# Performance work log

Measured on AMD Instinct MI355X. Metric: run time of the kernel, lower is better.

Reference implementation:

```python
import jax, jax.numpy as jnp
import numpy as np

EMPTY = -100.0
# class_relation_dict from init_kwargs (int keys)
CLASS_RELATIONS = {0: [1, 2], 1: [0, 3], 2: [4, 5], 3: [6, 7],
                   4: [0, 1], 5: [2, 3], 6: [4, 5], 7: [6, 0]}


def setup_inputs() -> dict:
    key = jax.random.key(0)
    B, C, D, H, W = 8, 8, 128, 128, 128
    x = jax.random.normal(key, (B, C, D, H, W), dtype=jnp.float32)
    # Make some class channels fully 'empty' so the mask-inference path fires
    # (randn alone never equals EMPTY exactly, which would make the op a no-op).
    x = x.at[:4, 0].set(EMPTY)
    x = x.at[2:6, 3].set(EMPTY)
    x = x.at[5:, 6].set(EMPTY)
    return {"x": x}


def reference(x):
    # x: [B, C, D, H, W]
    is_empty = x == EMPTY                       # [B, C, D, H, W] bool
    red_axes = tuple(range(2, x.ndim))
    all_empty = jnp.all(is_empty, axis=red_axes)   # [B, C] channel fully unlabeled
    has_empty = jnp.any(is_empty, axis=red_axes)   # [B, C] channel has any unlabeled voxel

    bshape = (-1,) + (1,) * (x.ndim - 2)  # broadcast [B] -> [B,1,1,1]
    out = jnp.full_like(x, EMPTY)
    for c, rel in CLASS_RELATIONS.items():
        # union of positives over related channels that are themselves fully labeled
        pos = jnp.zeros((x.shape[0],) + x.shape[2:], dtype=bool)
        for ind in rel:
            valid = (~has_empty[:, ind]).reshape(bshape)  # related channel fully labeled
            pos = pos | (valid & (x[:, ind] > 0))
        cond = all_empty[:, c].reshape(bshape) & pos
        out = out.at[:, c].set(jnp.where(cond, 0.0, EMPTY))
    return out
```

## Files before the change

### kernel.cpp

```cpp
#include <hip/hip_runtime.h>
#include <stdint.h>

#define EMPTY_VAL (-100.0f)

typedef float f4 __attribute__((ext_vector_type(4)));

constexpr int B = 8, C = 8;
constexpr int VOX       = 128 * 128 * 128;
constexpr int CH_VEC4   = VOX / 4;
constexpr int THREADS   = 256;
constexpr int ITERS     = 8;
constexpr int V4_PER_BLOCK    = THREADS * ITERS;
constexpr int BLOCKS_PER_BATCH = CH_VEC4 / V4_PER_BLOCK;
constexpr int GRID      = B * BLOCKS_PER_BATCH;

constexpr int REL0c[8] = {1, 0, 4, 6, 0, 2, 4, 6};
constexpr int REL1c[8] = {2, 3, 5, 7, 1, 3, 5, 0};

__global__ __launch_bounds__(THREADS) void mask_kernel(
    const float* __restrict__ x, uint32_t* __restrict__ mask,
    int* __restrict__ flagsE, int* __restrict__ flagsN) {
  const int b     = blockIdx.x / BLOCKS_PER_BATCH;
  const int chunk = blockIdx.x % BLOCKS_PER_BATCH;
  const int tid   = threadIdx.x;
  const size_t vb4 = (size_t)chunk * V4_PER_BLOCK;

  const f4* xb = reinterpret_cast<const f4*>(x) + (size_t)b * C * CH_VEC4;
  uint32_t* mb = mask + (size_t)b * CH_VEC4;

  uint32_t anyE = 0, anyN = 0;

  for (int it = 0; it < ITERS; ++it) {
    const size_t i4 = vb4 + (size_t)it * THREADS + tid;
    uint32_t m = 0;
#pragma unroll
    for (int c = 0; c < C; ++c) {
      const f4 v = __builtin_nontemporal_load(xb + ((size_t)c * CH_VEC4 + i4));
      uint32_t pos = (v.x > 0.f ? 0x00000001u : 0u) |
                     (v.y > 0.f ? 0x00000100u : 0u) |
                     (v.z > 0.f ? 0x00010000u : 0u) |
                     (v.w > 0.f ? 0x01000000u : 0u);
      m |= pos << c;
      const bool e0 = (v.x == EMPTY_VAL), e1 = (v.y == EMPTY_VAL);
      const bool e2 = (v.z == EMPTY_VAL), e3 = (v.w == EMPTY_VAL);
      if (e0 | e1 | e2 | e3)             anyE |= (1u << c);
      if ((!e0) | (!e1) | (!e2) | (!e3)) anyN |= (1u << c);
    }
    __builtin_nontemporal_store(m, mb + i4);
  }

#pragma unroll
  for (int o = 32; o > 0; o >>= 1) {
    anyE |= __shfl_xor((int)anyE, o);
    anyN |= __shfl_xor((int)anyN, o);
  }
  __shared__ int sE, sN;
  if (tid == 0) { sE = 0; sN = 0; }
  __syncthreads();
  if ((tid & 63) == 0) {
    if (anyE) atomicOr(&sE, (int)anyE);
    if (anyN) atomicOr(&sN, (int)anyN);
  }
  __syncthreads();
  if (tid == 0) {
    if (sE) atomicOr(&flagsE[b], sE);
    if (sN) atomicOr(&flagsN[b], sN);
  }
}

__global__ __launch_bounds__(THREADS) void emit_kernel(
    const uint32_t* __restrict__ mask, const int* __restrict__ flagsE,
    const int* __restrict__ flagsN, float* __restrict__ out) {
  const int b     = blockIdx.x / BLOCKS_PER_BATCH;
  const int chunk = blockIdx.x % BLOCKS_PER_BATCH;
  const int tid   = threadIdx.x;

  const int fE = flagsE[b], fN = flagsN[b];

  uint32_t relmask[C];
#pragma unroll
  for (int c = 0; c < C; ++c) {
    const bool all_empty = ((fN >> c) & 1) == 0;
    uint32_t rm = 0;
    if (all_empty) {
      if (((fE >> REL0c[c]) & 1) == 0) rm |= 1u << REL0c[c];
      if (((fE >> REL1c[c]) & 1) == 0) rm |= 1u << REL1c[c];
    }
    relmask[c] = rm * 0x01010101u;
  }

  const size_t vb4 = (size_t)chunk * V4_PER_BLOCK;
  const uint32_t* mb = mask + (size_t)b * CH_VEC4;
  f4* ob = reinterpret_cast<f4*>(out) + (size_t)b * C * CH_VEC4;

  for (int it = 0; it < ITERS; ++it) {
    const size_t i4 = vb4 + (size_t)it * THREADS + tid;
    const uint32_t m = mb[i4];
#pragma unroll
    for (int c = 0; c < C; ++c) {
      const uint32_t t = m & relmask[c];
      f4 r;
      r.x = (t & 0x000000ffu) ? 0.f : EMPTY_VAL;
      r.y = (t & 0x0000ff00u) ? 0.f : EMPTY_VAL;
      r.z = (t & 0x00ff0000u) ? 0.f : EMPTY_VAL;
      r.w = (t & 0xff000000u) ? 0.f : EMPTY_VAL;
      __builtin_nontemporal_store(r, ob + ((size_t)c * CH_VEC4 + i4));
    }
  }
}

constexpr int FB_V4_PER_THREAD = 16;
constexpr int FB_BLOCK_VEC4    = THREADS * FB_V4_PER_THREAD;
constexpr int FB_BLOCKS_PER_CH = CH_VEC4 / FB_BLOCK_VEC4;
constexpr int NCH              = B * C;
constexpr int FB_TOTAL_BLOCKS  = NCH * FB_BLOCKS_PER_CH;

__global__ __launch_bounds__(THREADS) void fb_flags_kernel(
    const float* __restrict__ x, int* __restrict__ flags) {
  const int blk   = blockIdx.x;
  const int ch    = blk / FB_BLOCKS_PER_CH;
  const int chunk = blk % FB_BLOCKS_PER_CH;
  const int tid   = threadIdx.x;
  const float4* p = reinterpret_cast<const float4*>(x) +
                    (size_t)ch * CH_VEC4 + (size_t)chunk * FB_BLOCK_VEC4;
  bool any_empty = false, any_nonempty = false;
#pragma unroll
  for (int i = 0; i < FB_V4_PER_THREAD; ++i) {
    float4 v = p[tid + i * THREADS];
    const bool e0 = (v.x == EMPTY_VAL), e1 = (v.y == EMPTY_VAL);
    const bool e2 = (v.z == EMPTY_VAL), e3 = (v.w == EMPTY_VAL);
    any_empty    |= (e0 | e1 | e2 | e3);
    any_nonempty |= (!e0 | !e1 | !e2 | !e3);
  }
  const bool we = __any(any_empty);
  const bool wn = __any(any_nonempty);
  __shared__ int s_e, s_n;
  if (tid == 0) { s_e = 0; s_n = 0; }
  __syncthreads();
  if ((tid & 63) == 0) {
    if (we) atomicOr(&s_e, 1);
    if (wn) atomicOr(&s_n, 1);
  }
  __syncthreads();
  if (tid == 0) {
    if (s_e) atomicOr(&flags[ch * 2 + 0], 1);
    if (s_n) atomicOr(&flags[ch * 2 + 1], 1);
  }
}

__global__ __launch_bounds__(THREADS) void fb_out_kernel(
    const float* __restrict__ x, const int* __restrict__ flags,
    float* __restrict__ out) {
  const int blk   = blockIdx.x;
  const int ch    = blk / FB_BLOCKS_PER_CH;
  const int chunk = blk % FB_BLOCKS_PER_CH;
  const int b     = ch >> 3;
  const int c     = ch & 7;
  const int tid   = threadIdx.x;
  const size_t base = (size_t)ch * CH_VEC4 + (size_t)chunk * FB_BLOCK_VEC4;
  float4* o = reinterpret_cast<float4*>(out) + base;
  const float4 empty4 = make_float4(EMPTY_VAL, EMPTY_VAL, EMPTY_VAL, EMPTY_VAL);
  const bool all_empty = (flags[ch * 2 + 1] == 0);
  if (!all_empty) {
#pragma unroll
    for (int i = 0; i < FB_V4_PER_THREAD; ++i) o[tid + i * THREADS] = empty4;
    return;
  }
  const int r0 = REL0c[c], r1 = REL1c[c];
  const bool v0 = (flags[(b * 8 + r0) * 2 + 0] == 0);
  const bool v1 = (flags[(b * 8 + r1) * 2 + 0] == 0);
  if (!v0 && !v1) {
#pragma unroll
    for (int i = 0; i < FB_V4_PER_THREAD; ++i) o[tid + i * THREADS] = empty4;
    return;
  }
  const float4* p0 = reinterpret_cast<const float4*>(x) +
                     ((size_t)(b * 8 + r0) * CH_VEC4 + (size_t)chunk * FB_BLOCK_VEC4);
  const float4* p1 = reinterpret_cast<const float4*>(x) +
                     ((size_t)(b * 8 + r1) * CH_VEC4 + (size_t)chunk * FB_BLOCK_VEC4);
  const float4 zero4 = make_float4(0.f, 0.f, 0.f, 0.f);
#pragma unroll
  for (int i = 0; i < FB_V4_PER_THREAD; ++i) {
    const int idx = tid + i * THREADS;
    const float4 a = v0 ? p0[idx] : zero4;
    const float4 q = v1 ? p1[idx] : zero4;
    float4 r;
    r.x = (a.x > 0.f || q.x > 0.f) ? 0.f : EMPTY_VAL;
    r.y = (a.y > 0.f || q.y > 0.f) ? 0.f : EMPTY_VAL;
    r.z = (a.z > 0.f || q.z > 0.f) ? 0.f : EMPTY_VAL;
    r.w = (a.w > 0.f || q.w > 0.f) ? 0.f : EMPTY_VAL;
    o[idx] = r;
  }
}

extern "C" void kernel_launch(void* const* d_in, const int* in_sizes, int n_in,
                              void* d_out, int out_size, void* d_ws, size_t ws_size,
                              hipStream_t stream) {
  const float* x = (const float*)d_in[0];
  float* out     = (float*)d_out;

  const size_t mask_bytes = (size_t)B * CH_VEC4 * sizeof(uint32_t);
  if (ws_size >= mask_bytes + 64) {
    uint32_t* mask = (uint32_t*)d_ws;
    int* flagsE    = (int*)((char*)d_ws + mask_bytes);
    int* flagsN    = flagsE + 8;
    (void)hipMemsetAsync(flagsE, 0, 16 * sizeof(int), stream);
    mask_kernel<<<GRID, THREADS, 0, stream>>>(x, mask, flagsE, flagsN);
    emit_kernel<<<GRID, THREADS, 0, stream>>>(mask, flagsE, flagsN, out);
  } else {
    int* flags = (int*)d_ws;
    (void)hipMemsetAsync(flags, 0, NCH * 2 * sizeof(int), stream);
    fb_flags_kernel<<<FB_TOTAL_BLOCKS, THREADS, 0, stream>>>(x, flags);
    fb_out_kernel<<<FB_TOTAL_BLOCKS, THREADS, 0, stream>>>(x, flags, out);
  }
}
```

Before: 215.7 us.

## Fuse mask and emit passes into one cooperative kernel with grid sync

```diff
diff --git a/kernel.cpp b/kernel.cpp
--- a/kernel.cpp
+++ b/kernel.cpp
@@ -1,4 +1,5 @@
 #include <hip/hip_runtime.h>
+#include <hip/hip_cooperative_groups.h>
 #include <stdint.h>
 
 #define EMPTY_VAL (-100.0f)
@@ -6,31 +7,32 @@
 typedef float f4 __attribute__((ext_vector_type(4)));
 
 constexpr int B = 8, C = 8;
-constexpr int VOX       = 128 * 128 * 128;
-constexpr int CH_VEC4   = VOX / 4;
-constexpr int THREADS   = 256;
-constexpr int ITERS     = 8;
-constexpr int V4_PER_BLOCK    = THREADS * ITERS;
-constexpr int BLOCKS_PER_BATCH = CH_VEC4 / V4_PER_BLOCK;
-constexpr int GRID      = B * BLOCKS_PER_BATCH;
+constexpr int VOX     = 128 * 128 * 128;
+constexpr int CH_VEC4 = VOX / 4;
+constexpr int THREADS = 256;
 
 constexpr int REL0c[8] = {1, 0, 4, 6, 0, 2, 4, 6};
 constexpr int REL1c[8] = {2, 3, 5, 7, 1, 3, 5, 0};
 
-__global__ __launch_bounds__(THREADS) void mask_kernel(
-    const float* __restrict__ x, uint32_t* __restrict__ mask,
-    int* __restrict__ flagsE, int* __restrict__ flagsN) {
-  const int b     = blockIdx.x / BLOCKS_PER_BATCH;
-  const int chunk = blockIdx.x % BLOCKS_PER_BATCH;
+constexpr int ITERS_F   = 16;
+constexpr int V4_BLK_F  = THREADS * ITERS_F;
+constexpr int BPB_F     = CH_VEC4 / V4_BLK_F;
+constexpr int GRID_F    = B * BPB_F;
+
+__global__ __launch_bounds__(THREADS, 4) void fused_kernel(
+    const float* __restrict__ x, int* __restrict__ flagsE,
+    int* __restrict__ flagsN, float* __restrict__ out) {
+  const int b     = blockIdx.x / BPB_F;
+  const int chunk = blockIdx.x % BPB_F;
   const int tid   = threadIdx.x;
-  const size_t vb4 = (size_t)chunk * V4_PER_BLOCK;
+  const size_t vb4 = (size_t)chunk * V4_BLK_F;
 
   const f4* xb = reinterpret_cast<const f4*>(x) + (size_t)b * C * CH_VEC4;
-  uint32_t* mb = mask + (size_t)b * CH_VEC4;
-
+
+  __shared__ uint32_t lds_m[V4_BLK_F];
   uint32_t anyE = 0, anyN = 0;
 
-  for (int it = 0; it < ITERS; ++it) {
+  for (int it = 0; it < ITERS_F; ++it) {
     const size_t i4 = vb4 + (size_t)it * THREADS + tid;
     uint32_t m = 0;
 #pragma unroll
@@ -46,7 +48,7 @@
       if (e0 | e1 | e2 | e3)             anyE |= (1u << c);
       if ((!e0) | (!e1) | (!e2) | (!e3)) anyN |= (1u << c);
     }
-    __builtin_nontemporal_store(m, mb + i4);
+    lds_m[it * THREADS + tid] = m;
   }
 
 #pragma unroll
@@ -66,16 +68,11 @@
     if (sE) atomicOr(&flagsE[b], sE);
     if (sN) atomicOr(&flagsN[b], sN);
   }
-}
-
-__global__ __launch_bounds__(THREADS) void emit_kernel(
-    const uint32_t* __restrict__ mask, const int* __restrict__ flagsE,
-    const int* __restrict__ flagsN, float* __restrict__ out) {
-  const int b     = blockIdx.x / BLOCKS_PER_BATCH;
-  const int chunk = blockIdx.x % BLOCKS_PER_BATCH;
-  const int tid   = threadIdx.x;
-
-  const int fE = flagsE[b], fN = flagsN[b];
+
+  cooperative_groups::this_grid().sync();
+
+  const int fE = __hip_atomic_load(&flagsE[b], __ATOMIC_RELAXED, __HIP_MEMORY_SCOPE_AGENT);
+  const int fN = __hip_atomic_load(&flagsN[b], __ATOMIC_RELAXED, __HIP_MEMORY_SCOPE_AGENT);
 
   uint32_t relmask[C];
 #pragma unroll
@@ -89,13 +86,10 @@
     relmask[c] = rm * 0x01010101u;
   }
 
-  const size_t vb4 = (size_t)chunk * V4_PER_BLOCK;
-  const uint32_t* mb = mask + (size_t)b * CH_VEC4;
   f4* ob = reinterpret_cast<f4*>(out) + (size_t)b * C * CH_VEC4;
-
-  for (int it = 0; it < ITERS; ++it) {
-    const size_t i4 = vb4 + (size_t)it * THREADS + tid;
-    const uint32_t m = mb[i4];
+  for (int it = 0; it < ITERS_F; ++it) {
+    const size_t i4 = vb4 + (size_t)it * THREADS + tid;
+    const uint32_t m = lds_m[it * THREADS + tid];
 #pragma unroll
     for (int c = 0; c < C; ++c) {
       const uint32_t t = m & relmask[c];
@@ -109,87 +103,97 @@
   }
 }
 
-constexpr int FB_V4_PER_THREAD = 16;
-constexpr int FB_BLOCK_VEC4    = THREADS * FB_V4_PER_THREAD;
-constexpr int FB_BLOCKS_PER_CH = CH_VEC4 / FB_BLOCK_VEC4;
-constexpr int NCH              = B * C;
-constexpr int FB_TOTAL_BLOCKS  = NCH * FB_BLOCKS_PER_CH;
-
-__global__ __launch_bounds__(THREADS) void fb_flags_kernel(
-    const float* __restrict__ x, int* __restrict__ flags) {
-  const int blk   = blockIdx.x;
-  const int ch    = blk / FB_BLOCKS_PER_CH;
-  const int chunk = blk % FB_BLOCKS_PER_CH;
+constexpr int ITERS    = 8;
+constexpr int V4_PER_BLOCK     = THREADS * ITERS;
+constexpr int BLOCKS_PER_BATCH = CH_VEC4 / V4_PER_BLOCK;
+constexpr int GRID     = B * BLOCKS_PER_BATCH;
+
+__global__ __launch_bounds__(THREADS) void mask_kernel(
+    const float* __restrict__ x, uint32_t* __restrict__ mask,
+    int* __restrict__ flagsE, int* __restrict__ flagsN) {
+  const int b     = blockIdx.x / BLOCKS_PER_BATCH;
+  const int chunk = blockIdx.x % BLOCKS_PER_BATCH;
   const int tid   = threadIdx.x;
-  const float4* p = reinterpret_cast<const float4*>(x) +
-                    (size_t)ch * CH_VEC4 + (size_t)chunk * FB_BLOCK_VEC4;
-  bool any_empty = false, any_nonempty = false;
-#pragma unroll
-  for (int i = 0; i < FB_V4_PER_THREAD; ++i) {
-    float4 v = p[tid + i * THREADS];
-    const bool e0 = (v.x == EMPTY_VAL), e1 = (v.y == EMPTY_VAL);
-    const bool e2 = (v.z == EMPTY_VAL), e3 = (v.w == EMPTY_VAL);
-    any_empty    |= (e0 | e1 | e2 | e3);
-    any_nonempty |= (!e0 | !e1 | !e2 | !e3);
-  }
-  const bool we = __any(any_empty);
-  const bool wn = __any(any_nonempty);
-  __shared__ int s_e, s_n;
-  if (tid == 0) { s_e = 0; s_n = 0; }
+  const size_t vb4 = (size_t)chunk * V4_PER_BLOCK;
+
+  const f4* xb = reinterpret_cast<const f4*>(x) + (size_t)b * C * CH_VEC4;
+  uint32_t* mb = mask + (size_t)b * CH_VEC4;
+
+  uint32_t anyE = 0, anyN = 0;
+  for (int it = 0; it < ITERS; ++it) {
+    const size_t i4 = vb4 + (size_t)it * THREADS + tid;
+    uint32_t m = 0;
+#pragma unroll
+    for (int c = 0; c < C; ++c) {
+      const f4 v = __builtin_nontemporal_load(xb + ((size_t)c * CH_VEC4 + i4));
+      uint32_t pos = (v.x > 0.f ? 0x00000001u : 0u) |
+                     (v.y > 0.f ? 0x00000100u : 0u) |
+                     (v.z > 0.f ? 0x00010000u : 0u) |
+                     (v.w > 0.f ? 0x01000000u : 0u);
+      m |= pos << c;
+      const bool e0 = (v.x == EMPTY_VAL), e1 = (v.y == EMPTY_VAL);
+      const bool e2 = (v.z == EMPTY_VAL), e3 = (v.w == EMPTY_VAL);
+      if (e0 | e1 | e2 | e3)             anyE |= (1u << c);
+      if ((!e0) | (!e1) | (!e2) | (!e3)) anyN |= (1u << c);
+    }
+    __builtin_nontemporal_store(m, mb + i4);
+  }
+#pragma unroll
+  for (int o = 32; o > 0; o >>= 1) {
+    anyE |= __shfl_xor((int)anyE, o);
+    anyN |= __shfl_xor((int)anyN, o);
+  }
+  __shared__ int sE, sN;
+  if (tid == 0) { sE = 0; sN = 0; }
   __syncthreads();
   if ((tid & 63) == 0) {
-    if (we) atomicOr(&s_e, 1);
-    if (wn) atomicOr(&s_n, 1);
+    if (anyE) atomicOr(&sE, (int)anyE);
+    if (anyN) atomicOr(&sN, (int)anyN);
   }
   __syncthreads();
   if (tid == 0) {
-    if (s_e) atomicOr(&flags[ch * 2 + 0], 1);
-    if (s_n) atomicOr(&flags[ch * 2 + 1], 1);
-  }
-}
-
-__global__ __launch_bounds__(THREADS) void fb_out_kernel(
-    const float* __restrict__ x, const int* __restrict__ flags,
-    float* __restrict__ out) {
-  const int blk   = blockIdx.x;
-  const int ch    = blk / FB_BLOCKS_PER_CH;
-  const int chunk = blk % FB_BLOCKS_PER_CH;
-  const int b     = ch >> 3;
-  const int c     = ch & 7;
+    if (sE) atomicOr(&flagsE[b], sE);
+    if (sN) atomicOr(&flagsN[b], sN);
+  }
+}
+
+__global__ __launch_bounds__(THREADS) void emit_kernel(
+    const uint32_t* __restrict__ mask, const int* __restrict__ flagsE,
+    const int* __restrict__ flagsN, float* __restrict__ out) {
+  const int b     = blockIdx.x / BLOCKS_PER_BATCH;
+  const int chunk = blockIdx.x % BLOCKS_PER_BATCH;
   const int tid   = threadIdx.x;
-  const size_t base = (size_t)ch * CH_VEC4 + (size_t)chunk * FB_BLOCK_VEC4;
-  float4* o = reinterpret_cast<float4*>(out) + base;
-  const float4 empty4 = make_float4(EMPTY_VAL, EMPTY_VAL, EMPTY_VAL, EMPTY_VAL);
-  const bool all_empty = (flags[ch * 2 + 1] == 0);
-  if (!all_empty) {
-#pragma unroll
-    for (int i = 0; i < FB_V4_PER_THREAD; ++i) o[tid + i * THREADS] = empty4;
-    return;
-  }
-  const int r0 = REL0c[c], r1 = REL1c[c];
-  const bool v0 = (flags[(b * 8 + r0) * 2 + 0] == 0);
-  const bool v1 = (flags[(b * 8 + r1) * 2 + 0] == 0);
-  if (!v0 && !v1) {
-#pragma unroll
-    for (int i = 0; i < FB_V4_PER_THREAD; ++i) o[tid + i * THREADS] = empty4;
-    return;
-  }
-  const float4* p0 = reinterpret_cast<const float4*>(x) +
-                     ((size_t)(b * 8 + r0) * CH_VEC4 + (size_t)chunk * FB_BLOCK_VEC4);
-  const float4* p1 = reinterpret_cast<const float4*>(x) +
-                     ((size_t)(b * 8 + r1) * CH_VEC4 + (size_t)chunk * FB_BLOCK_VEC4);
-  const float4 zero4 = make_float4(0.f, 0.f, 0.f, 0.f);
-#pragma unroll
-  for (int i = 0; i < FB_V4_PER_THREAD; ++i) {
-    const int idx = tid + i * THREADS;
-    const float4 a = v0 ? p0[idx] : zero4;
-    const float4 q = v1 ? p1[idx] : zero4;
-    float4 r;
-    r.x = (a.x > 0.f || q.x > 0.f) ? 0.f : EMPTY_VAL;
-    r.y = (a.y > 0.f || q.y > 0.f) ? 0.f : EMPTY_VAL;
-    r.z = (a.z > 0.f || q.z > 0.f) ? 0.f : EMPTY_VAL;
-    r.w = (a.w > 0.f || q.w > 0.f) ? 0.f : EMPTY_VAL;
-    o[idx] = r;
+
+  const int fE = flagsE[b], fN = flagsN[b];
+  uint32_t relmask[C];
+#pragma unroll
+  for (int c = 0; c < C; ++c) {
+    const bool all_empty = ((fN >> c) & 1) == 0;
+    uint32_t rm = 0;
+    if (all_empty) {
+      if (((fE >> REL0c[c]) & 1) == 0) rm |= 1u << REL0c[c];
+      if (((fE >> REL1c[c]) & 1) == 0) rm |= 1u << REL1c[c];
+    }
+    relmask[c] = rm * 0x01010101u;
+  }
+
+  const size_t vb4 = (size_t)chunk * V4_PER_BLOCK;
+  const uint32_t* mb = mask + (size_t)b * CH_VEC4;
+  f4* ob = reinterpret_cast<f4*>(out) + (size_t)b * C * CH_VEC4;
+
+  for (int it = 0; it < ITERS; ++it) {
+    const size_t i4 = vb4 + (size_t)it * THREADS + tid;
+    const uint32_t m = mb[i4];
+#pragma unroll
+    for (int c = 0; c < C; ++c) {
+      const uint32_t t = m & relmask[c];
+      f4 r;
+      r.x = (t & 0x000000ffu) ? 0.f : EMPTY_VAL;
+      r.y = (t & 0x0000ff00u) ? 0.f : EMPTY_VAL;
+      r.z = (t & 0x00ff0000u) ? 0.f : EMPTY_VAL;
+      r.w = (t & 0xff000000u) ? 0.f : EMPTY_VAL;
+      __builtin_nontemporal_store(r, ob + ((size_t)c * CH_VEC4 + i4));
+    }
   }
 }
 
@@ -200,17 +204,17 @@
   float* out     = (float*)d_out;
 
   const size_t mask_bytes = (size_t)B * CH_VEC4 * sizeof(uint32_t);
-  if (ws_size >= mask_bytes + 64) {
-    uint32_t* mask = (uint32_t*)d_ws;
-    int* flagsE    = (int*)((char*)d_ws + mask_bytes);
-    int* flagsN    = flagsE + 8;
-    (void)hipMemsetAsync(flagsE, 0, 16 * sizeof(int), stream);
-    mask_kernel<<<GRID, THREADS, 0, stream>>>(x, mask, flagsE, flagsN);
-    emit_kernel<<<GRID, THREADS, 0, stream>>>(mask, flagsE, flagsN, out);
-  } else {
-    int* flags = (int*)d_ws;
-    (void)hipMemsetAsync(flags, 0, NCH * 2 * sizeof(int), stream);
-    fb_flags_kernel<<<FB_TOTAL_BLOCKS, THREADS, 0, stream>>>(x, flags);
-    fb_out_kernel<<<FB_TOTAL_BLOCKS, THREADS, 0, stream>>>(x, flags, out);
-  }
-}
+  uint32_t* mask = (uint32_t*)d_ws;
+  int* flagsE    = (int*)((char*)d_ws + mask_bytes);
+  int* flagsN    = flagsE + 8;
+
+  (void)hipMemsetAsync(flagsE, 0, 16 * sizeof(int), stream);
+
+  void* args[] = {(void*)&x, (void*)&flagsE, (void*)&flagsN, (void*)&out};
+  hipError_t err = hipLaunchCooperativeKernel(
+      (const void*)fused_kernel, dim3(GRID_F), dim3(THREADS), args, 0, stream);
+  if (err == hipSuccess) return;
+
+  mask_kernel<<<GRID, THREADS, 0, stream>>>(x, mask, flagsE, flagsN);
+  emit_kernel<<<GRID, THREADS, 0, stream>>>(mask, flagsE, flagsN, out);
+}
```

Measured after the change: 313.6 us. 45.4% more time.
